# Performance work log

Hardware: AMD Instinct MI355X
Metric: run time of the kernel (lower is better)

Reference implementation:

```python
import jax, jax.numpy as jnp
import numpy as np
from jax import lax

B, M = 8192, 200
OUT_W = OUT_H = 16
NUM_LAYERS = 32
CNN_CH = 64
FLAT = CNN_CH * 2 * 2  # conv5/s3: 16->4, conv3/s1: 4->2
INPUT_SIZE = 128
HIDDEN = 128
CRITIC_H = 1024
ACTOR_H = 512
EMB_D = 16
NUM_ACTIONS = 100


def setup_inputs() -> dict:
    key = jax.random.key(0)
    ks = jax.random.split(key, 20)
    # token observations: [coord_byte, attr_index, attr_value] packed as int32
    coords = jax.random.randint(ks[0], (B, M), 0, 256)          # coord byte; 255 = invalid token
    attrs = jax.random.randint(ks[1], (B, M), 0, 40)            # some >= NUM_LAYERS -> masked
    vals = jax.random.randint(ks[2], (B, M), 0, 256)
    observations = jnp.stack([coords, attrs, vals], axis=-1).astype(jnp.int32)

    def lin(k, out_d, in_d, scale=None):
        s = scale if scale is not None else 1.0 / np.sqrt(in_d)
        return jax.random.uniform(k, (out_d, in_d), jnp.float32, -s, s)

    max_vec = jax.random.uniform(ks[3], (1, NUM_LAYERS, 1, 1), jnp.float32, 0.5, 30.0)
    cnn1_w = jax.random.normal(ks[4], (CNN_CH, NUM_LAYERS, 5, 5), jnp.float32) * 0.05
    cnn1_b = jnp.zeros((CNN_CH,), jnp.float32)
    cnn2_w = jax.random.normal(ks[5], (CNN_CH, CNN_CH, 3, 3), jnp.float32) * 0.05
    cnn2_b = jnp.zeros((CNN_CH,), jnp.float32)
    fc1_w = lin(ks[6], 128, FLAT); fc1_b = jnp.zeros((128,), jnp.float32)
    enc_w = lin(ks[7], INPUT_SIZE, 128); enc_b = jnp.zeros((INPUT_SIZE,), jnp.float32)
    critic1_w = lin(ks[8], CRITIC_H, HIDDEN); critic1_b = jnp.zeros((CRITIC_H,), jnp.float32)
    value_w = lin(ks[9], 1, CRITIC_H); value_b = jnp.zeros((1,), jnp.float32)
    actor1_w = lin(ks[10], ACTOR_H, HIDDEN); actor1_b = jnp.zeros((ACTOR_H,), jnp.float32)
    emb = jax.random.normal(ks[11], (NUM_ACTIONS, EMB_D), jnp.float32)
    action_emb = emb * (0.1 / jnp.max(jnp.abs(emb)))
    bound = 1.0 / np.sqrt(ACTOR_H)
    actor_W = jax.random.uniform(ks[12], (1, ACTOR_H, EMB_D), jnp.float32, -bound, bound)
    actor_bias = jax.random.uniform(ks[13], (1,), jnp.float32, -bound, bound)
    return dict(observations=observations, max_vec=max_vec,
                cnn1_w=cnn1_w, cnn1_b=cnn1_b, cnn2_w=cnn2_w, cnn2_b=cnn2_b,
                fc1_w=fc1_w, fc1_b=fc1_b, enc_w=enc_w, enc_b=enc_b,
                critic1_w=critic1_w, critic1_b=critic1_b, value_w=value_w, value_b=value_b,
                actor1_w=actor1_w, actor1_b=actor1_b, action_emb=action_emb,
                actor_W=actor_W, actor_bias=actor_bias)


def _encode_box(observations):
    # bit-unpack coord byte, mask, scatter into dense [B, L, W, H] box
    coords = observations[..., 0]                       # [B, M]
    x_idx = (coords >> 4) & 15
    y_idx = coords & 15
    atr_idx = observations[..., 1]
    atr_val = observations[..., 2].astype(jnp.float32)
    valid = (coords != 255) & (atr_idx < NUM_LAYERS)
    dim = OUT_W * OUT_H
    combined = atr_idx * dim + x_idx * OUT_H + y_idx    # [B, M]
    safe_idx = jnp.where(valid, combined, 0)
    safe_val = jnp.where(valid, atr_val, 0.0)
    box = jnp.zeros((observations.shape[0], NUM_LAYERS * dim), jnp.float32)
    box = box.at[jnp.arange(observations.shape[0])[:, None], safe_idx].set(safe_val)
    return box.reshape(-1, NUM_LAYERS, OUT_W, OUT_H)


def _conv(x, w, b, stride):
    y = lax.conv_general_dilated(x, w, (stride, stride), 'VALID',
                                 dimension_numbers=('NCHW', 'OIHW', 'NCHW'))
    return y + b[None, :, None, None]


def reference(observations, max_vec, cnn1_w, cnn1_b, cnn2_w, cnn2_b, fc1_w, fc1_b,
              enc_w, enc_b, critic1_w, critic1_b, value_w, value_b,
              actor1_w, actor1_b, action_emb, actor_W, actor_bias):
    box = _encode_box(observations)
    x = box / max_vec
    x = jax.nn.relu(_conv(x, cnn1_w, cnn1_b, 3))
    x = jax.nn.relu(_conv(x, cnn2_w, cnn2_b, 1))
    x = x.reshape(x.shape[0], -1)                       # [B, FLAT]
    x = jax.nn.relu(x @ fc1_w.T + fc1_b)
    hidden = jax.nn.relu(x @ enc_w.T + enc_b)           # [B, 128]
    # critic
    cf = jnp.tanh(hidden @ critic1_w.T + critic1_b)
    value = cf @ value_w.T + value_b                    # [B, 1]
    # bilinear actor (k=1: query is action-independent)
    af = jax.nn.relu(hidden @ actor1_w.T + actor1_b)    # [B, ACTOR_H]
    query = jnp.tanh(jnp.einsum('bh,he->be', af, actor_W[0]))
    logits = query @ action_emb[:NUM_ACTIONS].T + actor_bias  # [B, NUM_ACTIONS]
    return logits, value
```

## Files before the change

### kernel.cpp

```cpp
#include <hip/hip_runtime.h>
#include <math.h>

#define B_ 8192

typedef __attribute__((ext_vector_type(8))) short short8;
typedef __attribute__((ext_vector_type(4))) float f32x4;

__device__ unsigned short g_w1p[51200];
__device__ unsigned short g_w2p[36864];
__device__ unsigned short g_fc1hi[32768], g_fc1lo[32768];
__device__ unsigned short g_enchi[16384], g_enclo[16384];
__device__ unsigned short g_crp[131072];
__device__ unsigned short g_acp[65536];
__device__ unsigned short g_qWp[8192];
__device__ unsigned short g_ACT1hi[8192*1024];

__device__ __forceinline__ unsigned short f2bf(float v){
    unsigned u = __builtin_bit_cast(unsigned, v);
    unsigned r = (u + 0x7fffu + ((u >> 16) & 1u)) >> 16;
    return (unsigned short)r;
}
__device__ __forceinline__ float bf2f(unsigned short h){
    unsigned u = ((unsigned)h) << 16;
    return __builtin_bit_cast(float, u);
}
__device__ __forceinline__ void split_store(float v, unsigned short* hi, unsigned short* lo){
    unsigned short h = f2bf(v);
    *hi = h;
    *lo = f2bf(v - bf2f(h));
}

__global__ __launch_bounds__(256) void prep_kernel(
    const float* __restrict__ w1, const float* __restrict__ maxv,
    const float* __restrict__ w2, const float* __restrict__ fc1,
    const float* __restrict__ enc, const float* __restrict__ cr,
    const float* __restrict__ ac, const float* __restrict__ aW)
{
    int d = blockIdx.x * 256 + threadIdx.x;
    if (d < 51200){
        int n = d / 800, k = d - n*800;
        int l = k / 25;
        float v = w1[d] / maxv[l];
        int kc = k >> 5, kh = k & 31, ng = n >> 4, r = n & 15;
        int idx = ((kc*4 + ng)*16 + r)*32 + kh;
        g_w1p[idx] = f2bf(v);
        return;
    }
    d -= 51200;
    if (d < 36864){
        int oc = d / 576, k2 = d - oc*576;
        int kxy = k2 >> 6, ic = k2 & 63;
        float v = w2[oc*576 + ic*9 + kxy];
        int kc = k2 >> 6, ks = (k2 >> 5) & 1, kq = k2 & 31, nt = oc >> 4, r = oc & 15;
        int idx = (((kc*2 + ks)*4 + nt)*16 + r)*32 + kq;
        g_w2p[idx] = f2bf(v);
        return;
    }
    d -= 36864;
    if (d < 32768){
        int n = d >> 8, kp = d & 255;
        float v = fc1[n*256 + (kp & 63)*4 + (kp >> 6)];
        int idx = ((((n >> 4)*8) + (kp >> 5))*16 + (n & 15))*32 + (kp & 31);
        split_store(v, &g_fc1hi[idx], &g_fc1lo[idx]);
        return;
    }
    d -= 32768;
    if (d < 16384){
        int n = d >> 7, k = d & 127;
        int idx = ((((n >> 4)*4) + (k >> 5))*16 + (n & 15))*32 + (k & 31);
        split_store(enc[d], &g_enchi[idx], &g_enclo[idx]);
        return;
    }
    d -= 16384;
    if (d < 131072){
        int n = d >> 7, k = d & 127;
        int idx = ((((n >> 4)*4) + (k >> 5))*16 + (n & 15))*32 + (k & 31);
        g_crp[idx] = f2bf(cr[d]);
        return;
    }
    d -= 131072;
    if (d < 65536){
        int n = d >> 7, k = d & 127;
        int idx = ((((n >> 4)*4) + (k >> 5))*16 + (n & 15))*32 + (k & 31);
        g_acp[idx] = f2bf(ac[d]);
        return;
    }
    d -= 65536;
    {
        int e = d >> 9, j = d & 511;
        int idx = ((j >> 5)*16 + e)*32 + (j & 31);
        g_qWp[idx] = f2bf(aW[j*16 + e]);
    }
}

#define APITCH 808
__global__ __launch_bounds__(256, 3) void conv1_kernel(const int* __restrict__ obs,
                                                       const float* __restrict__ b1)
{
    const int b = blockIdx.x;
    const int tid = threadIdx.x;
    const int wave = tid >> 6, lane = tid & 63;
    const int l15 = lane & 15, lhi = lane >> 4;

    __shared__ unsigned short sA[32 * APITCH];
    int* wtab = (int*)sA;

    int   cells[2], xs[2], ys[2], ls[2];
    float vals[2];
    bool  valids[2], kept[2];
    #pragma unroll
    for (int u = 0; u < 2; u++){
        const int slot = tid + u*256;
        valids[u] = false; kept[u] = false; cells[u] = 0;
        if (slot < 400){
            const int si = (slot >= 200) ? 1 : 0;
            const int k  = slot - si*200;
            const int base = (b*2 + si)*600 + k*3;
            int coord = obs[base], atr = obs[base+1], val = obs[base+2];
            bool valid = (coord != 255) && (atr < 32);
            xs[u] = (coord >> 4) & 15;  ys[u] = coord & 15;  ls[u] = atr;
            cells[u] = valid ? (atr*256 + xs[u]*16 + ys[u]) : 0;
            vals[u]  = (float)val;
            valids[u] = valid;
        }
    }

    const unsigned short* Bhp = &g_w1p[wave*512 + l15*32 + lhi*8];
    short8 bh[25];
    #pragma unroll
    for (int kc = 0; kc < 25; kc++)
        bh[kc] = *(const short8*)&Bhp[kc*2048];

    if (tid < 200) wtab[cells[0]] = -1;
    __syncthreads();
    if (tid < 200) atomicMax(&wtab[cells[0]], tid);
    __syncthreads();
    if (tid < 200) kept[0] = (wtab[cells[0]] == tid);
    __syncthreads();
    if (tid >= 200) wtab[cells[0]] = -1;
    if (tid < 144)  wtab[cells[1]] = -1;
    __syncthreads();
    if (tid >= 200) atomicMax(&wtab[cells[0]], tid - 200);
    if (tid < 144)  atomicMax(&wtab[cells[1]], tid + 56);
    __syncthreads();
    if (tid >= 200) kept[0] = (wtab[cells[0]] == tid - 200);
    if (tid < 144)  kept[1] = (wtab[cells[1]] == tid + 56);
    __syncthreads();

    for (int i = tid; i < 4 * APITCH; i += 256)
        *(short8*)&sA[i * 8] = short8{0,0,0,0,0,0,0,0};
    __syncthreads();

    #pragma unroll
    for (int u = 0; u < 2; u++){
        const int slot = tid + u*256;
        if (slot < 400 && kept[u] && valids[u]){
            const int si = (slot >= 200) ? 1 : 0;
            const int x3 = xs[u]/3, rx = xs[u] - 3*x3;
            const int y3 = ys[u]/3, ry = ys[u] - 3*y3;
            const unsigned short hv = f2bf(vals[u]);
            #pragma unroll
            for (int d = 0; d < 4; d++){
                const int dxd = d >> 1, dyd = d & 1;
                const int ox = x3 - dxd, oy = y3 - dyd;
                const int wx = rx + 3*dxd, wy = ry + 3*dyd;
                if (((unsigned)ox <= 3u) && ((unsigned)oy <= 3u) && (wx < 5) && (wy < 5))
                    sA[(si*16 + ox*4 + oy)*APITCH + ls[u]*25 + wx*5 + wy] = hv;
            }
        }
    }
    __syncthreads();

    const int n = wave*16 + l15;
    const unsigned short* A0 = &sA[l15*APITCH + lhi*8];
    const unsigned short* A1 = &sA[(16 + l15)*APITCH + lhi*8];
    f32x4 acc0e = {0,0,0,0}, acc1e = {0,0,0,0};
    f32x4 acc0o = {0,0,0,0}, acc1o = {0,0,0,0};
    #pragma unroll
    for (int kc2 = 0; kc2 < 12; kc2++){
        const int kc = kc2*2;
        short8 a0e = *(const short8*)&A0[kc*32];
        short8 a1e = *(const short8*)&A1[kc*32];
        short8 a0o = *(const short8*)&A0[(kc+1)*32];
        short8 a1o = *(const short8*)&A1[(kc+1)*32];
        acc0e = __builtin_amdgcn_mfma_f32_16x16x32_bf16(a0e, bh[kc],   acc0e, 0, 0, 0);
        acc1e = __builtin_amdgcn_mfma_f32_16x16x32_bf16(a1e, bh[kc],   acc1e, 0, 0, 0);
        acc0o = __builtin_amdgcn_mfma_f32_16x16x32_bf16(a0o, bh[kc+1], acc0o, 0, 0, 0);
        acc1o = __builtin_amdgcn_mfma_f32_16x16x32_bf16(a1o, bh[kc+1], acc1o, 0, 0, 0);
    }
    {
        short8 a0e = *(const short8*)&A0[24*32];
        short8 a1e = *(const short8*)&A1[24*32];
        acc0e = __builtin_amdgcn_mfma_f32_16x16x32_bf16(a0e, bh[24], acc0e, 0, 0, 0);
        acc1e = __builtin_amdgcn_mfma_f32_16x16x32_bf16(a1e, bh[24], acc1e, 0, 0, 0);
    }
    f32x4 acc0, acc1;
    #pragma unroll
    for (int j = 0; j < 4; j++){ acc0[j] = acc0e[j] + acc0o[j]; acc1[j] = acc1e[j] + acc1o[j]; }

    const float bb = b1[n];
    #pragma unroll
    for (int j = 0; j < 4; j++){
        const int pos = lhi*4 + j;
        float v0 = fmaxf(acc0[j] + bb, 0.f);
        float v1 = fmaxf(acc1[j] + bb, 0.f);
        g_ACT1hi[(b*2    )*1024 + pos*64 + n] = f2bf(v0);
        g_ACT1hi[(b*2 + 1)*1024 + pos*64 + n] = f2bf(v1);
    }
}

__global__ __launch_bounds__(512, 4) void tail_kernel(
    const float* __restrict__ b2,   const float* __restrict__ fc1b,
    const float* __restrict__ encb, const float* __restrict__ crb,
    const float* __restrict__ vw,   const float* __restrict__ vb,
    const float* __restrict__ acb,  const float* __restrict__ emb,
    const float* __restrict__ abias, float* __restrict__ out)
{
    const int r0 = blockIdx.x * 16;
    const int tid = threadIdx.x, wave = tid >> 6, lane = tid & 63;
    const int l15 = lane & 15, lhi = lane >> 4;
    const int coff = l15*32 + lhi*8;

    __shared__ char smem[52736];
    unsigned short* sA1h = (unsigned short*)smem;
    unsigned short* sA1l = (unsigned short*)(smem + 8448);
    float*          qpart= (float*)smem;
    unsigned short* sXh  = (unsigned short*)(smem + 16896);
    unsigned short* sXl  = (unsigned short*)(smem + 21248);
    float* svred = (float*)(smem + 16896);
    float* sq    = (float*)(smem + 17408);
    float* semb  = (float*)(smem + 18496);
    unsigned short* sHh  = (unsigned short*)(smem + 25600);
    unsigned short* sHl  = (unsigned short*)(smem + 29952);
    unsigned short* cb   = (unsigned short*)(smem + 34304);
    unsigned short* sACT = (unsigned short*)(smem + 16896);

    {
        for (int u = tid; u < 2048; u += 512){
            const int row = u >> 7, c8 = (u & 127) * 8;
            *(short8*)&sACT[row*1032 + c8] = *(const short8*)&g_ACT1hi[(r0 + row)*1024 + c8];
        }
        __syncthreads();

        f32x4 c2acc[2] = {{0,0,0,0},{0,0,0,0}};
        const int tile0 = wave*2,     mt0 = tile0 >> 2, nt0 = tile0 & 3;
        const int tile1 = wave*2 + 1, mt1 = tile1 >> 2, nt1 = tile1 & 3;
        const int row0 = mt0*16 + l15, smp0 = row0 >> 2, px0 = (row0 >> 1) & 1, py0 = row0 & 1;
        const int row1 = mt1*16 + l15, smp1 = row1 >> 2, px1 = (row1 >> 1) & 1, py1 = row1 & 1;
        #pragma unroll
        for (int kc = 0; kc < 9; kc++){
            const int kx = kc / 3, ky = kc - 3*kx;
            const int cell0 = (px0 + kx)*4 + (py0 + ky);
            const int cell1 = (px1 + kx)*4 + (py1 + ky);
            #pragma unroll
            for (int ks = 0; ks < 2; ks++){
                const int kk = ks*32 + lhi*8;
                short8 a0 = *(const short8*)&sACT[smp0*1032 + cell0*64 + kk];
                short8 a1 = *(const short8*)&sACT[smp1*1032 + cell1*64 + kk];
                const short8 b0 = *(const short8*)&g_w2p[((kc*2 + ks)*4 + nt0)*512 + coff];
                const short8 b1 = *(const short8*)&g_w2p[((kc*2 + ks)*4 + nt1)*512 + coff];
                c2acc[0] = __builtin_amdgcn_mfma_f32_16x16x32_bf16(a0, b0, c2acc[0], 0, 0, 0);
                c2acc[1] = __builtin_amdgcn_mfma_f32_16x16x32_bf16(a1, b1, c2acc[1], 0, 0, 0);
            }
        }
        __syncthreads();
        #pragma unroll
        for (int wt = 0; wt < 2; wt++){
            const int tile = wave*2 + wt, mt = tile >> 2, nt = tile & 3;
            const int col = nt*16 + l15;
            const float bb = b2[col];
            #pragma unroll
            for (int j = 0; j < 4; j++){
                const int row = mt*16 + lhi*4 + j;
                float v = fmaxf(c2acc[wt][j] + bb, 0.f);
                unsigned short h = f2bf(v);
                const int ai = (row >> 2)*264 + (row & 3)*64 + col;
                sA1h[ai] = h;
                sA1l[ai] = f2bf(v - bf2f(h));
            }
        }
    }
    __syncthreads();

    {
        f32x4 acc = {0,0,0,0};
        const int n = wave*16 + l15;
        #pragma unroll
        for (int kk8 = 0; kk8 < 8; kk8++){
            const int kk = kk8*32 + lhi*8;
            short8 ah = *(const short8*)&sA1h[l15*264 + kk];
            short8 al = *(const short8*)&sA1l[l15*264 + kk];
            const short8 bh = *(const short8*)&g_fc1hi[(wave*8 + kk8)*512 + coff];
            const short8 bl = *(const short8*)&g_fc1lo[(wave*8 + kk8)*512 + coff];
            acc = __builtin_amdgcn_mfma_f32_16x16x32_bf16(ah, bh, acc, 0, 0, 0);
            acc = __builtin_amdgcn_mfma_f32_16x16x32_bf16(al, bh, acc, 0, 0, 0);
            acc = __builtin_amdgcn_mfma_f32_16x16x32_bf16(ah, bl, acc, 0, 0, 0);
        }
        __syncthreads();
        const float bb = fc1b[n];
        #pragma unroll
        for (int j = 0; j < 4; j++){
            const int row = lhi*4 + j;
            float v = fmaxf(acc[j] + bb, 0.f);
            unsigned short h = f2bf(v);
            sXh[row*136 + n] = h;
            sXl[row*136 + n] = f2bf(v - bf2f(h));
        }
    }
    __syncthreads();

    {
        f32x4 acc = {0,0,0,0};
        const int n = wave*16 + l15;
        #pragma unroll
        for (int kk4 = 0; kk4 < 4; kk4++){
            const int kk = kk4*32 + lhi*8;
            short8 ah = *(const short8*)&sXh[l15*136 + kk];
            short8 al = *(const short8*)&sXl[l15*136 + kk];
            const short8 bh = *(const short8*)&g_enchi[(wave*4 + kk4)*512 + coff];
            const short8 bl = *(const short8*)&g_enclo[(wave*4 + kk4)*512 + coff];
            acc = __builtin_amdgcn_mfma_f32_16x16x32_bf16(ah, bh, acc, 0, 0, 0);
            acc = __builtin_amdgcn_mfma_f32_16x16x32_bf16(al, bh, acc, 0, 0, 0);
            acc = __builtin_amdgcn_mfma_f32_16x16x32_bf16(ah, bl, acc, 0, 0, 0);
        }
        const float bb = encb[n];
        #pragma unroll
        for (int j = 0; j < 4; j++){
            const int row = lhi*4 + j;
            float v = fmaxf(acc[j] + bb, 0.f);
            unsigned short h = f2bf(v);
            sHh[row*136 + n] = h;
            sHl[row*136 + n] = f2bf(v - bf2f(h));
        }
    }
    __syncthreads();

    short8 Ah[4], Al[4];
    #pragma unroll
    for (int kk4 = 0; kk4 < 4; kk4++){
        const int kk = kk4*32 + lhi*8;
        Ah[kk4] = *(const short8*)&sHh[l15*136 + kk];
        Al[kk4] = *(const short8*)&sHl[l15*136 + kk];
    }

    {
        float vp[4] = {0,0,0,0};
        #pragma unroll
        for (int ntc = 0; ntc < 2; ntc++){
            f32x4 cacc[4];
            #pragma unroll
            for (int q = 0; q < 4; q++) cacc[q] = f32x4{0,0,0,0};
            #pragma unroll
            for (int q = 0; q < 4; q++){
                const int t = wave*8 + ntc*4 + q;
                #pragma unroll
                for (int kk4 = 0; kk4 < 4; kk4++){
                    const short8 bh = *(const short8*)&g_crp[(t*4 + kk4)*512 + coff];
                    cacc[q] = __builtin_amdgcn_mfma_f32_16x16x32_bf16(Ah[kk4], bh, cacc[q], 0, 0, 0);
                    cacc[q] = __builtin_amdgcn_mfma_f32_16x16x32_bf16(Al[kk4], bh, cacc[q], 0, 0, 0);
                }
            }
            #pragma unroll
            for (int q = 0; q < 4; q++){
                const int n = wave*128 + (ntc*4 + q)*16 + l15;
                const float w = vw[n], bb = crb[n];
                #pragma unroll
                for (int j = 0; j < 4; j++)
                    vp[j] += tanhf(cacc[q][j] + bb) * w;
            }
        }
        #pragma unroll
        for (int m = 1; m < 16; m <<= 1)
            #pragma unroll
            for (int j = 0; j < 4; j++) vp[j] += __shfl_xor(vp[j], m, 64);
        if (l15 == 0){
            #pragma unroll
            for (int j = 0; j < 4; j++)
                svred[wave*16 + lhi*4 + j] = vp[j];
        }
    }

    __syncthreads();
    f32x4 qacc = {0,0,0,0};
    {
        const int c = wave;
        f32x4 aacc[4];
        #pragma unroll
        for (int nt = 0; nt < 4; nt++) aacc[nt] = f32x4{0,0,0,0};
        #pragma unroll
        for (int kk4 = 0; kk4 < 4; kk4++){
            #pragma unroll
            for (int nt = 0; nt < 4; nt++){
                const int t = c*4 + nt;
                const short8 bh = *(const short8*)&g_acp[(t*4 + kk4)*512 + coff];
                aacc[nt] = __builtin_amdgcn_mfma_f32_16x16x32_bf16(Ah[kk4], bh, aacc[nt], 0, 0, 0);
                aacc[nt] = __builtin_amdgcn_mfma_f32_16x16x32_bf16(Al[kk4], bh, aacc[nt], 0, 0, 0);
            }
        }
        #pragma unroll
        for (int nt = 0; nt < 4; nt++){
            const int col = nt*16 + l15;
            const float bb = acb[c*64 + col];
            #pragma unroll
            for (int j = 0; j < 4; j++){
                const int row = lhi*4 + j;
                cb[(wave*16 + row)*72 + col] = f2bf(fmaxf(aacc[nt][j] + bb, 0.f));
            }
        }
        #pragma unroll
        for (int kk2 = 0; kk2 < 2; kk2++){
            const int kk = kk2*32 + lhi*8;
            const short8 qbh = *(const short8*)&g_qWp[(c*2 + kk2)*512 + coff];
            const short8 qah = *(const short8*)&cb[(wave*16 + l15)*72 + kk];
            qacc = __builtin_amdgcn_mfma_f32_16x16x32_bf16(qah, qbh, qacc, 0, 0, 0);
        }
    }
    #pragma unroll
    for (int j = 0; j < 4; j++)
        qpart[wave*256 + (lhi*4 + j)*16 + l15] = qacc[j];
    __syncthreads();

    if (tid < 16){
        float s = vb[0];
        #pragma unroll
        for (int w = 0; w < 8; w++) s += svred[w*16 + tid];
        out[B_*100 + r0 + tid] = s;
    }
    if (tid < 256){
        int row = tid >> 4, e = tid & 15;
        float s = 0.f;
        #pragma unroll
        for (int w = 0; w < 8; w++) s += qpart[w*256 + row*16 + e];
        sq[row*17 + e] = tanhf(s);
    }
    for (int k = tid; k < 1600; k += 512) semb[k] = emb[k];
    __syncthreads();
    for (int i = tid; i < 1600; i += 512){
        int row = i / 100, a = i - row*100;
        float s = abias[0];
        #pragma unroll
        for (int e = 0; e < 16; e++) s += sq[row*17 + e] * semb[a*16 + e];
        out[(r0 + row)*100 + a] = s;
    }
}

extern "C" void kernel_launch(void* const* d_in, const int* in_sizes, int n_in,
                              void* d_out, int out_size, void* d_ws, size_t ws_size,
                              hipStream_t stream) {
    const int*   obs   = (const int*)  d_in[0];
    const float* maxv  = (const float*)d_in[1];
    const float* w1    = (const float*)d_in[2];
    const float* b1    = (const float*)d_in[3];
    const float* w2    = (const float*)d_in[4];
    const float* b2    = (const float*)d_in[5];
    const float* fc1w  = (const float*)d_in[6];
    const float* fc1b  = (const float*)d_in[7];
    const float* encw  = (const float*)d_in[8];
    const float* encb  = (const float*)d_in[9];
    const float* crw   = (const float*)d_in[10];
    const float* crb   = (const float*)d_in[11];
    const float* vw    = (const float*)d_in[12];
    const float* vb    = (const float*)d_in[13];
    const float* acw   = (const float*)d_in[14];
    const float* acb   = (const float*)d_in[15];
    const float* emb   = (const float*)d_in[16];
    const float* aW    = (const float*)d_in[17];
    const float* abias = (const float*)d_in[18];
    float* out = (float*)d_out;

    prep_kernel<<<1336, 256, 0, stream>>>(w1, maxv, w2, fc1w, encw, crw, acw, aW);
    conv1_kernel<<<B_/2, 256, 0, stream>>>(obs, b1);
    tail_kernel<<<512, 512, 0, stream>>>(b2, fc1b, encb, crb, vw, vb, acb, emb, abias, out);
}
```

Measured before the change: 81.75 us.

## Split conv1 im2col into two K-passes to halve LDS and raise occupancy

The conv1 kernel now builds its im2col tile in shared memory in two halves over the reduction dimension (416 columns each, pitch 424) instead of all 800 at once. This shrinks the shared footprint to the 32KB hash table. It also streams the weight fragments from global memory per step instead of preloading all 25 into registers, and raises launch bounds from 3 to 5 blocks per CU. The aim is higher occupancy for better latency hiding. The cost is an extra zero-fill, scatter and barrier round, plus weight loads that now sit inside the MFMA loop.

Result: no change. 82.59 us (+1.0%).

```diff
diff --git a/kernel.cpp b/kernel.cpp
--- a/kernel.cpp
+++ b/kernel.cpp
@@ -93,8 +93,8 @@
     }
 }
 
-#define APITCH 808
-__global__ __launch_bounds__(256, 3) void conv1_kernel(const int* __restrict__ obs,
+#define APITCH2 424
+__global__ __launch_bounds__(256, 5) void conv1_kernel(const int* __restrict__ obs,
                                                        const float* __restrict__ b1)
 {
     const int b = blockIdx.x;
@@ -102,8 +102,8 @@
     const int wave = tid >> 6, lane = tid & 63;
     const int l15 = lane & 15, lhi = lane >> 4;
 
-    __shared__ unsigned short sA[32 * APITCH];
-    int* wtab = (int*)sA;
+    __shared__ int wtab[8192];
+    unsigned short* sA = (unsigned short*)wtab;
 
     int   cells[2], xs[2], ys[2], ls[2];
     float vals[2];
@@ -124,13 +124,6 @@
             valids[u] = valid;
         }
     }
-
-    const unsigned short* Bhp = &g_w1p[wave*512 + l15*32 + lhi*8];
-    short8 bh[25];
-    #pragma unroll
-    for (int kc = 0; kc < 25; kc++)
-        bh[kc] = *(const short8*)&Bhp[kc*2048];
-
     if (tid < 200) wtab[cells[0]] = -1;
     __syncthreads();
     if (tid < 200) atomicMax(&wtab[cells[0]], tid);
@@ -147,57 +140,66 @@
     if (tid < 144)  kept[1] = (wtab[cells[1]] == tid + 56);
     __syncthreads();
 
-    for (int i = tid; i < 4 * APITCH; i += 256)
-        *(short8*)&sA[i * 8] = short8{0,0,0,0,0,0,0,0};
-    __syncthreads();
-
-    #pragma unroll
-    for (int u = 0; u < 2; u++){
-        const int slot = tid + u*256;
-        if (slot < 400 && kept[u] && valids[u]){
-            const int si = (slot >= 200) ? 1 : 0;
-            const int x3 = xs[u]/3, rx = xs[u] - 3*x3;
-            const int y3 = ys[u]/3, ry = ys[u] - 3*y3;
-            const unsigned short hv = f2bf(vals[u]);
-            #pragma unroll
-            for (int d = 0; d < 4; d++){
-                const int dxd = d >> 1, dyd = d & 1;
-                const int ox = x3 - dxd, oy = y3 - dyd;
-                const int wx = rx + 3*dxd, wy = ry + 3*dyd;
-                if (((unsigned)ox <= 3u) && ((unsigned)oy <= 3u) && (wx < 5) && (wy < 5))
-                    sA[(si*16 + ox*4 + oy)*APITCH + ls[u]*25 + wx*5 + wy] = hv;
-            }
-        }
-    }
-    __syncthreads();
-
-    const int n = wave*16 + l15;
-    const unsigned short* A0 = &sA[l15*APITCH + lhi*8];
-    const unsigned short* A1 = &sA[(16 + l15)*APITCH + lhi*8];
     f32x4 acc0e = {0,0,0,0}, acc1e = {0,0,0,0};
     f32x4 acc0o = {0,0,0,0}, acc1o = {0,0,0,0};
-    #pragma unroll
-    for (int kc2 = 0; kc2 < 12; kc2++){
-        const int kc = kc2*2;
-        short8 a0e = *(const short8*)&A0[kc*32];
-        short8 a1e = *(const short8*)&A1[kc*32];
-        short8 a0o = *(const short8*)&A0[(kc+1)*32];
-        short8 a1o = *(const short8*)&A1[(kc+1)*32];
-        acc0e = __builtin_amdgcn_mfma_f32_16x16x32_bf16(a0e, bh[kc],   acc0e, 0, 0, 0);
-        acc1e = __builtin_amdgcn_mfma_f32_16x16x32_bf16(a1e, bh[kc],   acc1e, 0, 0, 0);
-        acc0o = __builtin_amdgcn_mfma_f32_16x16x32_bf16(a0o, bh[kc+1], acc0o, 0, 0, 0);
-        acc1o = __builtin_amdgcn_mfma_f32_16x16x32_bf16(a1o, bh[kc+1], acc1o, 0, 0, 0);
-    }
-    {
-        short8 a0e = *(const short8*)&A0[24*32];
-        short8 a1e = *(const short8*)&A1[24*32];
-        acc0e = __builtin_amdgcn_mfma_f32_16x16x32_bf16(a0e, bh[24], acc0e, 0, 0, 0);
-        acc1e = __builtin_amdgcn_mfma_f32_16x16x32_bf16(a1e, bh[24], acc1e, 0, 0, 0);
-    }
+    const unsigned short* Bhp = &g_w1p[wave*512 + l15*32 + lhi*8];
+    const unsigned short* A0 = &sA[l15*APITCH2 + lhi*8];
+    const unsigned short* A1 = &sA[(16 + l15)*APITCH2 + lhi*8];
+
+    #pragma unroll
+    for (int pass = 0; pass < 2; pass++){
+        for (int i = tid; i < 1696; i += 256)
+            *(short8*)&sA[i * 8] = short8{0,0,0,0,0,0,0,0};
+        __syncthreads();
+
+        #pragma unroll
+        for (int u = 0; u < 2; u++){
+            const int slot = tid + u*256;
+            if (slot < 400 && kept[u] && valids[u]){
+                const int si = (slot >= 200) ? 1 : 0;
+                const int x3 = xs[u]/3, rx = xs[u] - 3*x3;
+                const int y3 = ys[u]/3, ry = ys[u] - 3*y3;
+                const unsigned short hv = f2bf(vals[u]);
+                #pragma unroll
+                for (int d = 0; d < 4; d++){
+                    const int dxd = d >> 1, dyd = d & 1;
+                    const int ox = x3 - dxd, oy = y3 - dyd;
+                    const int wx = rx + 3*dxd, wy = ry + 3*dyd;
+                    if (((unsigned)ox <= 3u) && ((unsigned)oy <= 3u) && (wx < 5) && (wy < 5)){
+                        const int c = ls[u]*25 + wx*5 + wy;
+                        const bool inpass = (pass == 0) ? (c < 416) : (c >= 416);
+                        if (inpass)
+                            sA[(si*16 + ox*4 + oy)*APITCH2 + (c - pass*416)] = hv;
+                    }
+                }
+            }
+        }
+        __syncthreads();
+
+        const int kc0 = (pass == 0) ? 0 : 13;
+        const int kc1 = (pass == 0) ? 13 : 25;
+        #pragma unroll
+        for (int kc = kc0; kc < kc1; kc++){
+            const int kl = kc - kc0;
+            short8 a0 = *(const short8*)&A0[kl*32];
+            short8 a1 = *(const short8*)&A1[kl*32];
+            const short8 bb8 = *(const short8*)&Bhp[kc*2048];
+            if (kc & 1){
+                acc0o = __builtin_amdgcn_mfma_f32_16x16x32_bf16(a0, bb8, acc0o, 0, 0, 0);
+                acc1o = __builtin_amdgcn_mfma_f32_16x16x32_bf16(a1, bb8, acc1o, 0, 0, 0);
+            } else {
+                acc0e = __builtin_amdgcn_mfma_f32_16x16x32_bf16(a0, bb8, acc0e, 0, 0, 0);
+                acc1e = __builtin_amdgcn_mfma_f32_16x16x32_bf16(a1, bb8, acc1e, 0, 0, 0);
+            }
+        }
+        if (pass == 0) __syncthreads();
+    }
+
     f32x4 acc0, acc1;
     #pragma unroll
     for (int j = 0; j < 4; j++){ acc0[j] = acc0e[j] + acc0o[j]; acc1[j] = acc1e[j] + acc1o[j]; }
 
+    const int n = wave*16 + l15;
     const float bb = b1[n];
     #pragma unroll
     for (int j = 0; j < 4; j++){
```
